# Optimization experiments

Hardware: AMD Instinct MI355X
Metric: run time of the kernel (lower is better)

Reference implementation:

```python
import jax, jax.numpy as jnp
import numpy as np

DIM = 1024
HEADS = 16
DIM_HEADS = DIM // HEADS  # 64
DIM_HIDDEN = DIM_HEADS * HEADS


def setup_inputs() -> dict:
    key = jax.random.key(0)
    k1, k2, k3, k4, k5 = jax.random.split(key, 5)
    b, t = 2, 2048
    x = jax.random.normal(k1, (b, t, DIM), dtype=jnp.float32)
    # torch nn.Linear weights are [out_features, in_features]
    s = DIM ** -0.5
    W_q = jax.random.normal(k2, (DIM_HIDDEN, DIM), dtype=jnp.float32) * s
    W_kv = jax.random.normal(k3, (2 * DIM_HIDDEN, DIM), dtype=jnp.float32) * s
    W_out = jax.random.normal(k4, (DIM, DIM_HIDDEN), dtype=jnp.float32) * s
    b_out = jax.random.normal(k5, (DIM,), dtype=jnp.float32) * 0.01
    return {"x": x, "W_q": W_q, "W_kv": W_kv, "W_out": W_out, "b_out": b_out}


def reference(x, W_q, W_kv, W_out, b_out):
    b, t, d = x.shape
    h, e = HEADS, DIM_HEADS
    # projections (Linear: x @ W.T)
    q = jnp.einsum('btd,fd->btf', x, W_q)
    kv = jnp.einsum('btd,fd->btf', x, W_kv)
    k, v = jnp.split(kv, 2, axis=-1)
    # split heads -> (b, h, t, e)
    split = lambda z: z.reshape(b, t, h, e).transpose(0, 2, 1, 3)
    q, k, v = split(q), split(k), split(v)
    # scaled dot-product attention; original uses exp/sum/div softmax
    scores = jnp.einsum('bhqe,bhke->bhqk', q, k) * (e ** -0.5)
    attn = jax.nn.softmax(scores, axis=-1)
    out = jnp.einsum('bhqk,bhke->bhqe', attn, v)
    out = out.transpose(0, 2, 1, 3).reshape(b, t, h * e)
    return jnp.einsum('btf,df->btd', out, W_out) + b_out
```

## Files before the change

### kernel.cpp

```cpp
#include <hip/hip_runtime.h>
#include <hip/hip_bf16.h>

#define BB   2
#define TT   2048
#define DD   1024
#define HH   16
#define EE   64
#define BT   4096

typedef __attribute__((ext_vector_type(8))) short bf16x8;
typedef __attribute__((ext_vector_type(4))) float floatx4;
typedef __attribute__((ext_vector_type(16))) float floatx16;

__device__ __forceinline__ unsigned short f2bf(float f) {
  unsigned int x = __float_as_uint(f);
  x += 0x7fffu + ((x >> 16) & 1u);
  return (unsigned short)(x >> 16);
}
__device__ __forceinline__ unsigned int pack2u(float a, float b) {
  union { __hip_bfloat162 h; unsigned int u; } r;
  r.h = __float22bfloat162_rn(make_float2(a, b));
  return r.u;
}
__device__ __forceinline__ uint4 pack8(const float4& a, const float4& b) {
  union { uint4 u; __hip_bfloat162 h[4]; } r;
  r.h[0] = __float22bfloat162_rn(make_float2(a.x, a.y));
  r.h[1] = __float22bfloat162_rn(make_float2(a.z, a.w));
  r.h[2] = __float22bfloat162_rn(make_float2(b.x, b.y));
  r.h[3] = __float22bfloat162_rn(make_float2(b.z, b.w));
  return r.u;
}
__device__ __forceinline__ void ld16(unsigned short* lds, const unsigned short* g) {
  __builtin_amdgcn_global_load_lds(
      (const __attribute__((address_space(1))) unsigned int*)g,
      (__attribute__((address_space(3))) unsigned int*)lds, 16, 0, 0);
}

#define GX   524288
#define GWQ  131072
#define GWKV 262144
#define GWO  131072

__global__ __launch_bounds__(256) void convert_kernel(
    const float* __restrict__ X,  const float* __restrict__ Wq,
    const float* __restrict__ Wkv, const float* __restrict__ Wout,
    unsigned short* __restrict__ Xb, unsigned short* __restrict__ Wb,
    unsigned short* __restrict__ Wob) {
  int g = blockIdx.x * 256 + threadIdx.x;
  const float* src; unsigned short* dst; int gi;
  if (g < GX)                        { src = X;    dst = Xb;  gi = g; }
  else if ((g -= GX) < GWQ)          { src = Wq;   dst = Wb;  gi = g; }
  else if ((g -= GWQ) < GWKV)        { src = Wkv;  dst = Wb + (size_t)GWQ * 8; gi = g; }
  else                               { src = Wout; dst = Wob; gi = g - GWKV; }
  const float4* s4 = reinterpret_cast<const float4*>(src) + (size_t)gi * 2;
  float4 a = s4[0], b = s4[1];
  reinterpret_cast<uint4*>(dst)[gi] = pack8(a, b);
}

__global__ __launch_bounds__(256) void gemm_qkv_mfma(
    const unsigned short* __restrict__ Xb,
    const unsigned short* __restrict__ Wb,
    unsigned short* __restrict__ Qh,
    unsigned short* __restrict__ Kh,
    unsigned short* __restrict__ Vt) {
  __shared__ __align__(16) unsigned short As[128 * 64];
  __shared__ __align__(16) unsigned short Bs[128 * 64];
  const int tid  = threadIdx.x;
  const int lane = tid & 63, w = tid >> 6;
  const int wm = w >> 1, wn = w & 1;
  const int q = lane >> 4, c = lane & 15;
  const int bm0 = blockIdx.y * 128;
  const int bn0 = blockIdx.x * 128;
  const unsigned short* Ag = Xb + (size_t)bm0 * DD;
  const unsigned short* Bg = Wb + (size_t)bn0 * DD;

  floatx4 acc[4][4];
#pragma unroll
  for (int i = 0; i < 4; ++i)
#pragma unroll
    for (int j = 0; j < 4; ++j) acc[i][j] = (floatx4){0.f, 0.f, 0.f, 0.f};

  int prow[4], pch[4];
#pragma unroll
  for (int t = 0; t < 4; ++t) {
    int s = (w * 4 + t) * 64 + lane;
    prow[t] = s >> 3;
    pch[t]  = (s & 7) ^ (prow[t] & 7);
  }
  int aoff[4][2], boff[4][2];
#pragma unroll
  for (int i = 0; i < 4; ++i)
#pragma unroll
    for (int h = 0; h < 2; ++h) {
      aoff[i][h] = (wm * 64 + i * 16 + c) * 64 + (((q + h * 4) ^ (c & 7)) << 3);
      boff[i][h] = (wn * 64 + i * 16 + c) * 64 + (((q + h * 4) ^ (c & 7)) << 3);
    }

  for (int kk = 0; kk < DD; kk += 64) {
    __syncthreads();
#pragma unroll
    for (int t = 0; t < 4; ++t) {
      int i = w * 4 + t;
      ld16(&As[i * 512], &Ag[(size_t)prow[t] * DD + kk + pch[t] * 8]);
      ld16(&Bs[i * 512], &Bg[(size_t)prow[t] * DD + kk + pch[t] * 8]);
    }
    __syncthreads();
    bf16x8 af[4][2], bfr[4][2];
#pragma unroll
    for (int i = 0; i < 4; ++i)
#pragma unroll
      for (int h = 0; h < 2; ++h) {
        af[i][h]  = *reinterpret_cast<const bf16x8*>(&As[aoff[i][h]]);
        bfr[i][h] = *reinterpret_cast<const bf16x8*>(&Bs[boff[i][h]]);
      }
#pragma unroll
    for (int i = 0; i < 4; ++i)
#pragma unroll
      for (int j = 0; j < 4; ++j) {
        acc[i][j] = __builtin_amdgcn_mfma_f32_16x16x32_bf16(af[i][0], bfr[j][0], acc[i][j], 0, 0, 0);
        acc[i][j] = __builtin_amdgcn_mfma_f32_16x16x32_bf16(af[i][1], bfr[j][1], acc[i][j], 0, 0, 0);
      }
  }

  const int region = bn0 >> 10;
  const float scl = (region == 0) ? 0.125f : 1.0f;
#pragma unroll
  for (int i = 0; i < 4; ++i) {
#pragma unroll
    for (int j = 0; j < 4; ++j) {
#pragma unroll
      for (int reg = 0; reg < 4; ++reg) {
        int m = bm0 + wm * 64 + i * 16 + q * 4 + reg;
        int n = bn0 + wn * 64 + j * 16 + c;
        int nb = n & 1023;
        int h = nb >> 6, e = nb & 63;
        int b = m >> 11, t = m & 2047;
        unsigned short v = f2bf(acc[i][j][reg] * scl);
        if (region == 0)      Qh[((size_t)((b * HH + h) * TT + t)) * EE + e] = v;
        else if (region == 1) Kh[((size_t)((b * HH + h) * TT + t)) * EE + e] = v;
        else                  Vt[((size_t)(b * HH + h)) * EE * TT + (size_t)e * TT + t] = v;
      }
    }
  }
}

__global__ __launch_bounds__(128) void attn_kernel(
    const unsigned short* __restrict__ Qh,
    const unsigned short* __restrict__ Kh,
    const unsigned short* __restrict__ Vtg,
    unsigned short* __restrict__ Aw) {
  __shared__ __align__(16) unsigned short Ks[2][64 * 64];
  __shared__ __align__(16) unsigned short Vs[2][64 * 64];

  const int tid  = threadIdx.x;
  const int lane = tid & 63;
  const int w    = tid >> 6;
  const int n31  = lane & 31;
  const int g    = lane >> 5;

  const int qt = blockIdx.x;
  const int bh = blockIdx.y;
  const size_t base = (size_t)bh * TT * EE;
  const unsigned short* Qp = Qh + base + (size_t)(qt * 128 + w * 64) * EE;
  const unsigned short* Kp = Kh + base;
  const unsigned short* Vp = Vtg + base;

  bf16x8 qf[2][4];
#pragma unroll
  for (int s = 0; s < 2; ++s)
#pragma unroll
    for (int kc = 0; kc < 4; ++kc)
      qf[s][kc] = *reinterpret_cast<const bf16x8*>(
          &Qp[(size_t)(s * 32 + n31) * EE + kc * 16 + g * 8]);

  int srow[4], sch[4];
#pragma unroll
  for (int t = 0; t < 4; ++t) {
    int s = (t * 2 + w) * 64 + lane;
    srow[t] = s >> 3;
    sch[t]  = (s & 7) ^ (srow[t] & 7);
  }

  floatx16 o_acc[2][2];
  o_acc[0][0] = (floatx16)(0.0f); o_acc[0][1] = (floatx16)(0.0f);
  o_acc[1][0] = (floatx16)(0.0f); o_acc[1][1] = (floatx16)(0.0f);
  float l_sum[2] = {0.0f, 0.0f};

#pragma unroll
  for (int t = 0; t < 4; ++t) {
    ld16(&Ks[0][(t * 2 + w) * 512], &Kp[(size_t)srow[t] * EE + sch[t] * 8]);
    ld16(&Vs[0][(t * 2 + w) * 512], &Vp[(size_t)srow[t] * TT + sch[t] * 8]);
  }

  for (int kt = 0; kt < 32; ++kt) {
    const int p  = kt & 1;
    const int nk = (kt + 1) & 31;
#pragma unroll
    for (int t = 0; t < 4; ++t) {
      ld16(&Ks[p ^ 1][(t * 2 + w) * 512], &Kp[(size_t)(nk * 64 + srow[t]) * EE + sch[t] * 8]);
      ld16(&Vs[p ^ 1][(t * 2 + w) * 512], &Vp[(size_t)srow[t] * TT + nk * 64 + sch[t] * 8]);
    }
    asm volatile("s_waitcnt vmcnt(8)" ::: "memory");
    asm volatile("s_barrier" ::: "memory");

    const unsigned short* Kb = Ks[p];
    const unsigned short* Vb = Vs[p];

#pragma unroll
    for (int s = 0; s < 2; ++s) {
      floatx16 sacc[2];
      sacc[0] = (floatx16)(0.0f);
      sacc[1] = (floatx16)(0.0f);
#pragma unroll
      for (int nt = 0; nt < 2; ++nt) {
        const int krow = nt * 32 + n31;
#pragma unroll
        for (int kc = 0; kc < 4; ++kc) {
          const int swch = (kc * 2 + g) ^ (krow & 7);
          bf16x8 kf = *reinterpret_cast<const bf16x8*>(&Kb[krow * 64 + swch * 8]);
          sacc[nt] = __builtin_amdgcn_mfma_f32_32x32x16_bf16(kf, qf[s][kc], sacc[nt], 0, 0, 0);
        }
      }
      unsigned int pp[2][8] __attribute__((aligned(16)));
#pragma unroll
      for (int nt = 0; nt < 2; ++nt)
#pragma unroll
        for (int r = 0; r < 8; ++r) {
          float e0 = __expf(sacc[nt][2 * r]);
          float e1 = __expf(sacc[nt][2 * r + 1]);
          l_sum[s] += e0 + e1;
          pp[nt][r] = pack2u(e0, e1);
        }
#pragma unroll
      for (int nt = 0; nt < 2; ++nt)
#pragma unroll
        for (int kcp = 0; kcp < 2; ++kcp) {
          union { unsigned int u[4]; bf16x8 v; } pf;
          pf.u[0] = pp[nt][4 * kcp + 0]; pf.u[1] = pp[nt][4 * kcp + 1];
          pf.u[2] = pp[nt][4 * kcp + 2]; pf.u[3] = pp[nt][4 * kcp + 3];
#pragma unroll
          for (int eh = 0; eh < 2; ++eh) {
            const int vrow = eh * 32 + n31;
            const int c0 = (nt * 4 + 2 * kcp)     ^ (vrow & 7);
            const int c1 = (nt * 4 + 2 * kcp + 1) ^ (vrow & 7);
            uint2 v0 = *reinterpret_cast<const uint2*>(&Vb[vrow * 64 + c0 * 8 + g * 4]);
            uint2 v1 = *reinterpret_cast<const uint2*>(&Vb[vrow * 64 + c1 * 8 + g * 4]);
            union { unsigned int u[4]; bf16x8 v; } vf;
            vf.u[0] = v0.x; vf.u[1] = v0.y; vf.u[2] = v1.x; vf.u[3] = v1.y;
            o_acc[s][eh] = __builtin_amdgcn_mfma_f32_32x32x16_bf16(pf.v, vf.v, o_acc[s][eh], 0, 0, 0);
          }
        }
    }
    asm volatile("s_barrier" ::: "memory");
  }

  l_sum[0] += __shfl_xor(l_sum[0], 32, 64);
  l_sum[1] += __shfl_xor(l_sum[1], 32, 64);

  const int b = bh >> 4, h = bh & 15;
#pragma unroll
  for (int s = 0; s < 2; ++s) {
    float linv[16];
#pragma unroll
    for (int reg = 0; reg < 16; ++reg) {
      int qrl = (reg & 3) + 8 * (reg >> 2) + 4 * g;
      linv[reg] = 1.0f / __shfl(l_sum[s], qrl, 64);
    }
#pragma unroll
    for (int eh = 0; eh < 2; ++eh) {
      int e = eh * 32 + n31;
#pragma unroll
      for (int reg = 0; reg < 16; ++reg) {
        int qrl = (reg & 3) + 8 * (reg >> 2) + 4 * g;
        int t = qt * 128 + w * 64 + s * 32 + qrl;
        Aw[((size_t)(b * TT + t)) * DD + h * EE + e] = f2bf(o_acc[s][eh][reg] * linv[reg]);
      }
    }
  }
}

__global__ __launch_bounds__(256) void gemm_out_mfma(
    const unsigned short* __restrict__ A,
    const unsigned short* __restrict__ Wob,
    const float* __restrict__ bias,
    float* __restrict__ out) {
  __shared__ __align__(16) unsigned short As[128 * 64];
  __shared__ __align__(16) unsigned short Bs[64 * 64];
  const int tid  = threadIdx.x;
  const int lane = tid & 63, w = tid >> 6;
  const int wm = w >> 1, wn = w & 1;
  const int q = lane >> 4, c = lane & 15;
  const int bm0 = blockIdx.y * 128;
  const int bn0 = blockIdx.x * 64;
  const unsigned short* Ag = A + (size_t)bm0 * DD;
  const unsigned short* Bg = Wob + (size_t)bn0 * DD;

  floatx4 acc[4][2];
#pragma unroll
  for (int i = 0; i < 4; ++i)
#pragma unroll
    for (int j = 0; j < 2; ++j) acc[i][j] = (floatx4){0.f, 0.f, 0.f, 0.f};

  int parow[4], pach[4];
#pragma unroll
  for (int t = 0; t < 4; ++t) {
    int s = (w * 4 + t) * 64 + lane;
    parow[t] = s >> 3;
    pach[t]  = (s & 7) ^ (parow[t] & 7);
  }
  int pbrow[2], pbch[2];
#pragma unroll
  for (int t = 0; t < 2; ++t) {
    int s = (w * 2 + t) * 64 + lane;
    pbrow[t] = s >> 3;
    pbch[t]  = (s & 7) ^ (pbrow[t] & 7);
  }

  for (int kk = 0; kk < DD; kk += 64) {
    __syncthreads();
#pragma unroll
    for (int t = 0; t < 4; ++t)
      ld16(&As[(w * 4 + t) * 512], &Ag[(size_t)parow[t] * DD + kk + pach[t] * 8]);
#pragma unroll
    for (int t = 0; t < 2; ++t)
      ld16(&Bs[(w * 2 + t) * 512], &Bg[(size_t)pbrow[t] * DD + kk + pbch[t] * 8]);
    __syncthreads();
    bf16x8 af[4][2], bfr[2][2];
#pragma unroll
    for (int h = 0; h < 2; ++h) {
      int ksw = ((q + h * 4) ^ (c & 7)) << 3;
#pragma unroll
      for (int i = 0; i < 4; ++i)
        af[i][h] = *reinterpret_cast<const bf16x8*>(&As[(wm * 64 + i * 16 + c) * 64 + ksw]);
#pragma unroll
      for (int j = 0; j < 2; ++j)
        bfr[j][h] = *reinterpret_cast<const bf16x8*>(&Bs[(wn * 32 + j * 16 + c) * 64 + ksw]);
    }
#pragma unroll
    for (int i = 0; i < 4; ++i)
#pragma unroll
      for (int j = 0; j < 2; ++j) {
        acc[i][j] = __builtin_amdgcn_mfma_f32_16x16x32_bf16(af[i][0], bfr[j][0], acc[i][j], 0, 0, 0);
        acc[i][j] = __builtin_amdgcn_mfma_f32_16x16x32_bf16(af[i][1], bfr[j][1], acc[i][j], 0, 0, 0);
      }
  }

#pragma unroll
  for (int i = 0; i < 4; ++i) {
#pragma unroll
    for (int j = 0; j < 2; ++j) {
      int n = bn0 + wn * 32 + j * 16 + c;
      float bv = bias[n];
#pragma unroll
      for (int reg = 0; reg < 4; ++reg) {
        int m = bm0 + wm * 64 + i * 16 + q * 4 + reg;
        out[(size_t)m * DD + n] = acc[i][j][reg] + bv;
      }
    }
  }
}

extern "C" void kernel_launch(void* const* d_in, const int* in_sizes, int n_in,
                              void* d_out, int out_size, void* d_ws, size_t ws_size,
                              hipStream_t stream) {
  const float* X    = (const float*)d_in[0];
  const float* Wq   = (const float*)d_in[1];
  const float* Wkv  = (const float*)d_in[2];
  const float* Wout = (const float*)d_in[3];
  const float* bout = (const float*)d_in[4];
  float* out = (float*)d_out;

  unsigned short* Qh  = (unsigned short*)d_ws;
  unsigned short* Kh  = Qh + (size_t)BT * DD;
  unsigned short* Vt  = Kh + (size_t)BT * DD;
  unsigned short* Aw  = Vt + (size_t)BT * DD;
  unsigned short* Xb  = Aw;
  unsigned short* Wb  = Aw + (size_t)BT * DD;
  unsigned short* Wob = Wb + (size_t)3 * 1024 * DD;

  convert_kernel<<<dim3(4096), 256, 0, stream>>>(X, Wq, Wkv, Wout, Xb, Wb, Wob);
  gemm_qkv_mfma<<<dim3(24, 32), 256, 0, stream>>>(Xb, Wb, Qh, Kh, Vt);
  attn_kernel<<<dim3(16, 32), 128, 0, stream>>>(Qh, Kh, Vt, Aw);
  gemm_out_mfma<<<dim3(16, 32), 256, 0, stream>>>(Aw, Wob, bout, out);
}
```

Baseline: 205.0 us.

## Split attention KV range across two wave pairs and fold log2e into Q scale

```diff
diff --git a/kernel.cpp b/kernel.cpp
--- a/kernel.cpp
+++ b/kernel.cpp
@@ -123,7 +123,7 @@
   }
 
   const int region = bn0 >> 10;
-  const float scl = (region == 0) ? 0.125f : 1.0f;
+  const float scl = (region == 0) ? 0.18033688011112042f : 1.0f;
 #pragma unroll
   for (int i = 0; i < 4; ++i) {
 #pragma unroll
@@ -144,26 +144,32 @@
   }
 }
 
-__global__ __launch_bounds__(128) void attn_kernel(
+#define CHUNK 16
+
+__global__ __launch_bounds__(256) void attn_kernel(
     const unsigned short* __restrict__ Qh,
     const unsigned short* __restrict__ Kh,
     const unsigned short* __restrict__ Vtg,
     unsigned short* __restrict__ Aw) {
-  __shared__ __align__(16) unsigned short Ks[2][64 * 64];
-  __shared__ __align__(16) unsigned short Vs[2][64 * 64];
+  __shared__ __align__(16) unsigned short smem[32768];
 
   const int tid  = threadIdx.x;
   const int lane = tid & 63;
   const int w    = tid >> 6;
+  const int wv   = w & 1;
+  const int p2   = w >> 1;
   const int n31  = lane & 31;
   const int g    = lane >> 5;
 
   const int qt = blockIdx.x;
   const int bh = blockIdx.y;
   const size_t base = (size_t)bh * TT * EE;
-  const unsigned short* Qp = Qh + base + (size_t)(qt * 128 + w * 64) * EE;
+  const unsigned short* Qp = Qh + base + (size_t)(qt * 128 + wv * 64) * EE;
   const unsigned short* Kp = Kh + base;
   const unsigned short* Vp = Vtg + base;
+
+  unsigned short* Kbuf = smem + p2 * 16384;
+  unsigned short* Vbuf = smem + p2 * 16384 + 8192;
 
   bf16x8 qf[2][4];
 #pragma unroll
@@ -176,7 +182,7 @@
   int srow[4], sch[4];
 #pragma unroll
   for (int t = 0; t < 4; ++t) {
-    int s = (t * 2 + w) * 64 + lane;
+    int s = (t * 2 + wv) * 64 + lane;
     srow[t] = s >> 3;
     sch[t]  = (s & 7) ^ (srow[t] & 7);
   }
@@ -186,25 +192,39 @@
   o_acc[1][0] = (floatx16)(0.0f); o_acc[1][1] = (floatx16)(0.0f);
   float l_sum[2] = {0.0f, 0.0f};
 
+  const int kt0 = p2 * CHUNK;
 #pragma unroll
   for (int t = 0; t < 4; ++t) {
-    ld16(&Ks[0][(t * 2 + w) * 512], &Kp[(size_t)srow[t] * EE + sch[t] * 8]);
-    ld16(&Vs[0][(t * 2 + w) * 512], &Vp[(size_t)srow[t] * TT + sch[t] * 8]);
-  }
-
-  for (int kt = 0; kt < 32; ++kt) {
+    ld16(&Kbuf[(t * 2 + wv) * 512], &Kp[(size_t)(kt0 * 64 + srow[t]) * EE + sch[t] * 8]);
+    ld16(&Vbuf[(t * 2 + wv) * 512], &Vp[(size_t)srow[t] * TT + kt0 * 64 + sch[t] * 8]);
+  }
+
+  for (int kt = 0; kt < CHUNK; ++kt) {
     const int p  = kt & 1;
-    const int nk = (kt + 1) & 31;
+    const int gt = kt0 + ((kt + 1) & (CHUNK - 1));
 #pragma unroll
     for (int t = 0; t < 4; ++t) {
-      ld16(&Ks[p ^ 1][(t * 2 + w) * 512], &Kp[(size_t)(nk * 64 + srow[t]) * EE + sch[t] * 8]);
-      ld16(&Vs[p ^ 1][(t * 2 + w) * 512], &Vp[(size_t)srow[t] * TT + nk * 64 + sch[t] * 8]);
+      ld16(&Kbuf[(p ^ 1) * 4096 + (t * 2 + wv) * 512],
+           &Kp[(size_t)(gt * 64 + srow[t]) * EE + sch[t] * 8]);
+      ld16(&Vbuf[(p ^ 1) * 4096 + (t * 2 + wv) * 512],
+           &Vp[(size_t)srow[t] * TT + gt * 64 + sch[t] * 8]);
     }
     asm volatile("s_waitcnt vmcnt(8)" ::: "memory");
     asm volatile("s_barrier" ::: "memory");
 
-    const unsigned short* Kb = Ks[p];
-    const unsigned short* Vb = Vs[p];
+    const unsigned short* Kb = Kbuf + p * 4096;
+    const unsigned short* Vb = Vbuf + p * 4096;
+
+    bf16x8 kf[2][4];
+#pragma unroll
+    for (int nt = 0; nt < 2; ++nt) {
+      const int krow = nt * 32 + n31;
+#pragma unroll
+      for (int kc = 0; kc < 4; ++kc) {
+        const int swch = (kc * 2 + g) ^ (krow & 7);
+        kf[nt][kc] = *reinterpret_cast<const bf16x8*>(&Kb[krow * 64 + swch * 8]);
+      }
+    }
 
 #pragma unroll
     for (int s = 0; s < 2; ++s) {
@@ -212,25 +232,22 @@
       sacc[0] = (floatx16)(0.0f);
       sacc[1] = (floatx16)(0.0f);
 #pragma unroll
-      for (int nt = 0; nt < 2; ++nt) {
-        const int krow = nt * 32 + n31;
-#pragma unroll
-        for (int kc = 0; kc < 4; ++kc) {
-          const int swch = (kc * 2 + g) ^ (krow & 7);
-          bf16x8 kf = *reinterpret_cast<const bf16x8*>(&Kb[krow * 64 + swch * 8]);
-          sacc[nt] = __builtin_amdgcn_mfma_f32_32x32x16_bf16(kf, qf[s][kc], sacc[nt], 0, 0, 0);
-        }
-      }
+      for (int nt = 0; nt < 2; ++nt)
+#pragma unroll
+        for (int kc = 0; kc < 4; ++kc)
+          sacc[nt] = __builtin_amdgcn_mfma_f32_32x32x16_bf16(kf[nt][kc], qf[s][kc], sacc[nt], 0, 0, 0);
+
       unsigned int pp[2][8] __attribute__((aligned(16)));
 #pragma unroll
       for (int nt = 0; nt < 2; ++nt)
 #pragma unroll
         for (int r = 0; r < 8; ++r) {
-          float e0 = __expf(sacc[nt][2 * r]);
-          float e1 = __expf(sacc[nt][2 * r + 1]);
+          float e0 = __builtin_amdgcn_exp2f(sacc[nt][2 * r]);
+          float e1 = __builtin_amdgcn_exp2f(sacc[nt][2 * r + 1]);
           l_sum[s] += e0 + e1;
           pp[nt][r] = pack2u(e0, e1);
         }
+
 #pragma unroll
       for (int nt = 0; nt < 2; ++nt)
 #pragma unroll
@@ -257,24 +274,43 @@
   l_sum[0] += __shfl_xor(l_sum[0], 32, 64);
   l_sum[1] += __shfl_xor(l_sum[1], 32, 64);
 
-  const int b = bh >> 4, h = bh & 15;
-#pragma unroll
-  for (int s = 0; s < 2; ++s) {
-    float linv[16];
-#pragma unroll
-    for (int reg = 0; reg < 16; ++reg) {
-      int qrl = (reg & 3) + 8 * (reg >> 2) + 4 * g;
-      linv[reg] = 1.0f / __shfl(l_sum[s], qrl, 64);
-    }
-#pragma unroll
-    for (int eh = 0; eh < 2; ++eh) {
-      int e = eh * 32 + n31;
+  __syncthreads();
+  float* fb = (float*)smem;
+  if (p2 == 1) {
+#pragma unroll
+    for (int s = 0; s < 2; ++s) {
+#pragma unroll
+      for (int eh = 0; eh < 2; ++eh)
+#pragma unroll
+        for (int reg = 0; reg < 16; ++reg) {
+          int qrl = (reg & 3) + 8 * (reg >> 2) + 4 * g;
+          fb[wv * 4224 + (s * 32 + qrl) * 66 + eh * 32 + n31] = o_acc[s][eh][reg];
+        }
+      if (g == 0) fb[8448 + wv * 64 + s * 32 + n31] = l_sum[s];
+    }
+  }
+  __syncthreads();
+  if (p2 == 0) {
+    const int b = bh >> 4, h = bh & 15;
+#pragma unroll
+    for (int s = 0; s < 2; ++s) {
+      float linv[16];
 #pragma unroll
       for (int reg = 0; reg < 16; ++reg) {
         int qrl = (reg & 3) + 8 * (reg >> 2) + 4 * g;
-        int t = qt * 128 + w * 64 + s * 32 + qrl;
-        Aw[((size_t)(b * TT + t)) * DD + h * EE + e] = f2bf(o_acc[s][eh][reg] * linv[reg]);
-      }
+        float lown = __shfl(l_sum[s], qrl, 64);
+        float lpar = fb[8448 + wv * 64 + s * 32 + qrl];
+        linv[reg] = 1.0f / (lown + lpar);
+      }
+#pragma unroll
+      for (int eh = 0; eh < 2; ++eh)
+#pragma unroll
+        for (int reg = 0; reg < 16; ++reg) {
+          int qrl = (reg & 3) + 8 * (reg >> 2) + 4 * g;
+          float o = o_acc[s][eh][reg] + fb[wv * 4224 + (s * 32 + qrl) * 66 + eh * 32 + n31];
+          int t = qt * 128 + wv * 64 + s * 32 + qrl;
+          Aw[((size_t)(b * TT + t)) * DD + h * EE + eh * 32 + n31] = f2bf(o * linv[reg]);
+        }
     }
   }
 }
@@ -380,6 +416,6 @@
 
   convert_kernel<<<dim3(4096), 256, 0, stream>>>(X, Wq, Wkv, Wout, Xb, Wb, Wob);
   gemm_qkv_mfma<<<dim3(24, 32), 256, 0, stream>>>(Xb, Wb, Qh, Kh, Vt);
-  attn_kernel<<<dim3(16, 32), 128, 0, stream>>>(Qh, Kh, Vt, Aw);
+  attn_kernel<<<dim3(16, 32), 256, 0, stream>>>(Qh, Kh, Vt, Aw);
   gemm_out_mfma<<<dim3(16, 32), 256, 0, stream>>>(Aw, Wob, bout, out);
 }
```

After: 200.7 us. 2.1% less time.

## Use four waves per attention block and fold log2e into Q scale for exp2

Applied to the files above, without the earlier changes.

```diff
diff --git a/kernel.cpp b/kernel.cpp
--- a/kernel.cpp
+++ b/kernel.cpp
@@ -123,7 +123,7 @@
   }
 
   const int region = bn0 >> 10;
-  const float scl = (region == 0) ? 0.125f : 1.0f;
+  const float scl = (region == 0) ? 0.18033688011112042f : 1.0f;
 #pragma unroll
   for (int i = 0; i < 4; ++i) {
 #pragma unroll
@@ -144,13 +144,13 @@
   }
 }
 
-__global__ __launch_bounds__(128) void attn_kernel(
+__global__ __launch_bounds__(256) void attn_kernel(
     const unsigned short* __restrict__ Qh,
     const unsigned short* __restrict__ Kh,
     const unsigned short* __restrict__ Vtg,
     unsigned short* __restrict__ Aw) {
-  __shared__ __align__(16) unsigned short Ks[2][64 * 64];
-  __shared__ __align__(16) unsigned short Vs[2][64 * 64];
+  __shared__ __align__(16) unsigned short Ks[2][4096];
+  __shared__ __align__(16) unsigned short Vs[2][4096];
 
   const int tid  = threadIdx.x;
   const int lane = tid & 63;
@@ -161,122 +161,114 @@
   const int qt = blockIdx.x;
   const int bh = blockIdx.y;
   const size_t base = (size_t)bh * TT * EE;
-  const unsigned short* Qp = Qh + base + (size_t)(qt * 128 + w * 64) * EE;
+  const unsigned short* Qp = Qh + base + (size_t)(qt * 128 + w * 32) * EE;
   const unsigned short* Kp = Kh + base;
   const unsigned short* Vp = Vtg + base;
 
-  bf16x8 qf[2][4];
-#pragma unroll
-  for (int s = 0; s < 2; ++s)
-#pragma unroll
-    for (int kc = 0; kc < 4; ++kc)
-      qf[s][kc] = *reinterpret_cast<const bf16x8*>(
-          &Qp[(size_t)(s * 32 + n31) * EE + kc * 16 + g * 8]);
-
-  int srow[4], sch[4];
-#pragma unroll
-  for (int t = 0; t < 4; ++t) {
-    int s = (t * 2 + w) * 64 + lane;
+  bf16x8 qf[4];
+#pragma unroll
+  for (int kc = 0; kc < 4; ++kc)
+    qf[kc] = *reinterpret_cast<const bf16x8*>(
+        &Qp[(size_t)n31 * EE + kc * 16 + g * 8]);
+
+  int srow[2], sch[2];
+#pragma unroll
+  for (int t = 0; t < 2; ++t) {
+    int s = (t * 4 + w) * 64 + lane;
     srow[t] = s >> 3;
     sch[t]  = (s & 7) ^ (srow[t] & 7);
   }
 
-  floatx16 o_acc[2][2];
-  o_acc[0][0] = (floatx16)(0.0f); o_acc[0][1] = (floatx16)(0.0f);
-  o_acc[1][0] = (floatx16)(0.0f); o_acc[1][1] = (floatx16)(0.0f);
-  float l_sum[2] = {0.0f, 0.0f};
-
-#pragma unroll
-  for (int t = 0; t < 4; ++t) {
-    ld16(&Ks[0][(t * 2 + w) * 512], &Kp[(size_t)srow[t] * EE + sch[t] * 8]);
-    ld16(&Vs[0][(t * 2 + w) * 512], &Vp[(size_t)srow[t] * TT + sch[t] * 8]);
+  floatx16 o_acc[2];
+  o_acc[0] = (floatx16)(0.0f);
+  o_acc[1] = (floatx16)(0.0f);
+  float l_sum = 0.0f;
+
+#pragma unroll
+  for (int t = 0; t < 2; ++t) {
+    ld16(&Ks[0][(t * 4 + w) * 512], &Kp[(size_t)srow[t] * EE + sch[t] * 8]);
+    ld16(&Vs[0][(t * 4 + w) * 512], &Vp[(size_t)srow[t] * TT + sch[t] * 8]);
   }
 
   for (int kt = 0; kt < 32; ++kt) {
     const int p  = kt & 1;
     const int nk = (kt + 1) & 31;
 #pragma unroll
-    for (int t = 0; t < 4; ++t) {
-      ld16(&Ks[p ^ 1][(t * 2 + w) * 512], &Kp[(size_t)(nk * 64 + srow[t]) * EE + sch[t] * 8]);
-      ld16(&Vs[p ^ 1][(t * 2 + w) * 512], &Vp[(size_t)srow[t] * TT + nk * 64 + sch[t] * 8]);
-    }
-    asm volatile("s_waitcnt vmcnt(8)" ::: "memory");
+    for (int t = 0; t < 2; ++t) {
+      ld16(&Ks[p ^ 1][(t * 4 + w) * 512], &Kp[(size_t)(nk * 64 + srow[t]) * EE + sch[t] * 8]);
+      ld16(&Vs[p ^ 1][(t * 4 + w) * 512], &Vp[(size_t)srow[t] * TT + nk * 64 + sch[t] * 8]);
+    }
+    asm volatile("s_waitcnt vmcnt(4)" ::: "memory");
     asm volatile("s_barrier" ::: "memory");
 
     const unsigned short* Kb = Ks[p];
     const unsigned short* Vb = Vs[p];
 
-#pragma unroll
-    for (int s = 0; s < 2; ++s) {
-      floatx16 sacc[2];
-      sacc[0] = (floatx16)(0.0f);
-      sacc[1] = (floatx16)(0.0f);
-#pragma unroll
-      for (int nt = 0; nt < 2; ++nt) {
-        const int krow = nt * 32 + n31;
-#pragma unroll
-        for (int kc = 0; kc < 4; ++kc) {
-          const int swch = (kc * 2 + g) ^ (krow & 7);
-          bf16x8 kf = *reinterpret_cast<const bf16x8*>(&Kb[krow * 64 + swch * 8]);
-          sacc[nt] = __builtin_amdgcn_mfma_f32_32x32x16_bf16(kf, qf[s][kc], sacc[nt], 0, 0, 0);
+    floatx16 sacc[2];
+    sacc[0] = (floatx16)(0.0f);
+    sacc[1] = (floatx16)(0.0f);
+#pragma unroll
+    for (int nt = 0; nt < 2; ++nt) {
+      const int krow = nt * 32 + n31;
+#pragma unroll
+      for (int kc = 0; kc < 4; ++kc) {
+        const int swch = (kc * 2 + g) ^ (krow & 7);
+        bf16x8 kf = *reinterpret_cast<const bf16x8*>(&Kb[krow * 64 + swch * 8]);
+        sacc[nt] = __builtin_amdgcn_mfma_f32_32x32x16_bf16(kf, qf[kc], sacc[nt], 0, 0, 0);
+      }
+    }
+
+    unsigned int pp[2][8] __attribute__((aligned(16)));
+#pragma unroll
+    for (int nt = 0; nt < 2; ++nt)
+#pragma unroll
+      for (int r = 0; r < 8; ++r) {
+        float e0 = __builtin_amdgcn_exp2f(sacc[nt][2 * r]);
+        float e1 = __builtin_amdgcn_exp2f(sacc[nt][2 * r + 1]);
+        l_sum += e0 + e1;
+        pp[nt][r] = pack2u(e0, e1);
+      }
+
+#pragma unroll
+    for (int nt = 0; nt < 2; ++nt)
+#pragma unroll
+      for (int kcp = 0; kcp < 2; ++kcp) {
+        union { unsigned int u[4]; bf16x8 v; } pf;
+        pf.u[0] = pp[nt][4 * kcp + 0]; pf.u[1] = pp[nt][4 * kcp + 1];
+        pf.u[2] = pp[nt][4 * kcp + 2]; pf.u[3] = pp[nt][4 * kcp + 3];
+#pragma unroll
+        for (int eh = 0; eh < 2; ++eh) {
+          const int vrow = eh * 32 + n31;
+          const int c0 = (nt * 4 + 2 * kcp)     ^ (vrow & 7);
+          const int c1 = (nt * 4 + 2 * kcp + 1) ^ (vrow & 7);
+          uint2 v0 = *reinterpret_cast<const uint2*>(&Vb[vrow * 64 + c0 * 8 + g * 4]);
+          uint2 v1 = *reinterpret_cast<const uint2*>(&Vb[vrow * 64 + c1 * 8 + g * 4]);
+          union { unsigned int u[4]; bf16x8 v; } vf;
+          vf.u[0] = v0.x; vf.u[1] = v0.y; vf.u[2] = v1.x; vf.u[3] = v1.y;
+          o_acc[eh] = __builtin_amdgcn_mfma_f32_32x32x16_bf16(pf.v, vf.v, o_acc[eh], 0, 0, 0);
         }
       }
-      unsigned int pp[2][8] __attribute__((aligned(16)));
-#pragma unroll
-      for (int nt = 0; nt < 2; ++nt)
-#pragma unroll
-        for (int r = 0; r < 8; ++r) {
-          float e0 = __expf(sacc[nt][2 * r]);
-          float e1 = __expf(sacc[nt][2 * r + 1]);
-          l_sum[s] += e0 + e1;
-          pp[nt][r] = pack2u(e0, e1);
-        }
-#pragma unroll
-      for (int nt = 0; nt < 2; ++nt)
-#pragma unroll
-        for (int kcp = 0; kcp < 2; ++kcp) {
-          union { unsigned int u[4]; bf16x8 v; } pf;
-          pf.u[0] = pp[nt][4 * kcp + 0]; pf.u[1] = pp[nt][4 * kcp + 1];
-          pf.u[2] = pp[nt][4 * kcp + 2]; pf.u[3] = pp[nt][4 * kcp + 3];
-#pragma unroll
-          for (int eh = 0; eh < 2; ++eh) {
-            const int vrow = eh * 32 + n31;
-            const int c0 = (nt * 4 + 2 * kcp)     ^ (vrow & 7);
-            const int c1 = (nt * 4 + 2 * kcp + 1) ^ (vrow & 7);
-            uint2 v0 = *reinterpret_cast<const uint2*>(&Vb[vrow * 64 + c0 * 8 + g * 4]);
-            uint2 v1 = *reinterpret_cast<const uint2*>(&Vb[vrow * 64 + c1 * 8 + g * 4]);
-            union { unsigned int u[4]; bf16x8 v; } vf;
-            vf.u[0] = v0.x; vf.u[1] = v0.y; vf.u[2] = v1.x; vf.u[3] = v1.y;
-            o_acc[s][eh] = __builtin_amdgcn_mfma_f32_32x32x16_bf16(pf.v, vf.v, o_acc[s][eh], 0, 0, 0);
-          }
-        }
-    }
     asm volatile("s_barrier" ::: "memory");
   }
 
-  l_sum[0] += __shfl_xor(l_sum[0], 32, 64);
-  l_sum[1] += __shfl_xor(l_sum[1], 32, 64);
+  l_sum += __shfl_xor(l_sum, 32, 64);
 
   const int b = bh >> 4, h = bh & 15;
-#pragma unroll
-  for (int s = 0; s < 2; ++s) {
-    float linv[16];
+  float linv[16];
+#pragma unroll
+  for (int reg = 0; reg < 16; ++reg) {
+    int qrl = (reg & 3) + 8 * (reg >> 2) + 4 * g;
+    linv[reg] = 1.0f / __shfl(l_sum, qrl, 64);
+  }
+#pragma unroll
+  for (int eh = 0; eh < 2; ++eh)
 #pragma unroll
     for (int reg = 0; reg < 16; ++reg) {
       int qrl = (reg & 3) + 8 * (reg >> 2) + 4 * g;
-      linv[reg] = 1.0f / __shfl(l_sum[s], qrl, 64);
-    }
-#pragma unroll
-    for (int eh = 0; eh < 2; ++eh) {
-      int e = eh * 32 + n31;
-#pragma unroll
-      for (int reg = 0; reg < 16; ++reg) {
-        int qrl = (reg & 3) + 8 * (reg >> 2) + 4 * g;
-        int t = qt * 128 + w * 64 + s * 32 + qrl;
-        Aw[((size_t)(b * TT + t)) * DD + h * EE + e] = f2bf(o_acc[s][eh][reg] * linv[reg]);
-      }
-    }
-  }
+      int t = qt * 128 + w * 32 + qrl;
+      Aw[((size_t)(b * TT + t)) * DD + h * EE + eh * 32 + n31] =
+          f2bf(o_acc[eh][reg] * linv[reg]);
+    }
 }
 
 __global__ __launch_bounds__(256) void gemm_out_mfma(
@@ -380,6 +372,6 @@
 
   convert_kernel<<<dim3(4096), 256, 0, stream>>>(X, Wq, Wkv, Wout, Xb, Wb, Wob);
   gemm_qkv_mfma<<<dim3(24, 32), 256, 0, stream>>>(Xb, Wb, Qh, Kh, Vt);
-  attn_kernel<<<dim3(16, 32), 128, 0, stream>>>(Qh, Kh, Vt, Aw);
+  attn_kernel<<<dim3(16, 32), 256, 0, stream>>>(Qh, Kh, Vt, Aw);
   gemm_out_mfma<<<dim3(16, 32), 256, 0, stream>>>(Aw, Wob, bout, out);
 }
```

Measured after the change: 201.2 us. Within noise of the previous version (-1.9%).
